# Kernel optimization log

Measured on AMD Instinct MI355X. Metric: run time of the kernel, lower is better.

Reference implementation:

```python
import jax, jax.numpy as jnp
import numpy as np

N_NODES = 50000
N_EDGES = 1600000
IN_CH = 128
OUT_CH = 128


def setup_inputs() -> dict:
    key = jax.random.key(0)
    k1, k2, k3, k4, k5 = jax.random.split(key, 5)
    x = jax.random.normal(k1, (N_NODES, IN_CH), dtype=jnp.float32)
    # edge_index[0] = destination (row), edge_index[1] = source (col)
    edge_index = jax.random.randint(k2, (2, N_EDGES), 0, N_NODES, dtype=jnp.int64)
    # Linear parameters (PyTorch default init: U(-1/sqrt(fan_in), 1/sqrt(fan_in)))
    bound = 1.0 / np.sqrt(IN_CH)
    W = jax.random.uniform(k3, (OUT_CH, IN_CH), dtype=jnp.float32, minval=-bound, maxval=bound)
    b = jax.random.uniform(k4, (OUT_CH,), dtype=jnp.float32, minval=-bound, maxval=bound)
    return {"x": x, "edge_index": edge_index, "W": W, "b": b}


def reference(x, edge_index, W, b) -> jnp.ndarray:
    # Linear projection: h = x @ W^T + b  -> [N, OUT_CH]
    h = jnp.einsum("nd,od->no", x, W) + b
    # spmm sum aggregation: out[dst] = sum_{edges e: dst(e)=dst} h[src(e)]
    dst = edge_index[0]
    src = edge_index[1]
    out = jax.ops.segment_sum(h[src], dst, num_segments=N_NODES)
    return out
```

## Files before the change

### kernel.cpp

```cpp
#include <hip/hip_runtime.h>

constexpr int N  = 50000;
constexpr int E  = 1600000;
constexpr int CH = 128;

constexpr int BSZ  = 64;
constexpr int NB   = (N + BSZ - 1) / BSZ;
constexpr int CAP  = 2560;
constexpr int PBLK = 256;
constexpr int EPB  = E / PBLK;
constexpr int GEMM_BLOCKS = N / 16;

constexpr size_t H_OFF     = 0;
constexpr size_t H_SZ      = (size_t)N * CH * 2;
constexpr size_t PAIRS_OFF = H_OFF + H_SZ;
constexpr size_t PAIRS_SZ  = (size_t)NB * CAP * 4;
constexpr size_t GCUR_OFF  = PAIRS_OFF + PAIRS_SZ;
constexpr size_t GCUR_SZ   = 3328;
constexpr size_t REQUIRED  = GCUR_OFF + GCUR_SZ;
constexpr size_t FB_REQUIRED = H_SZ;

static __device__ __forceinline__ ushort f2bf(float f) {
    unsigned u = __float_as_uint(f);
    return (ushort)((u + 0x7fffu + ((u >> 16) & 1u)) >> 16);
}
static __device__ __forceinline__ float bf_lo(unsigned u) { return __uint_as_float(u << 16); }
static __device__ __forceinline__ float bf_hi(unsigned u) { return __uint_as_float(u & 0xffff0000u); }

typedef __attribute__((ext_vector_type(8))) short bf16x8;
typedef __attribute__((ext_vector_type(4))) float f32x4;

static __device__ __forceinline__ void gemm_body(int gb, int tid,
                                                 const float* __restrict__ x,
                                                 const float* __restrict__ W,
                                                 const float* __restrict__ bias,
                                                 ushort* __restrict__ h) {
    const int m    = tid & 15;
    const int q    = (tid >> 4) & 3;
    const int wave = tid >> 6;
    const int r0   = gb * 16;
    const int c0   = wave * 32;

    const float* xrow = x + (size_t)(r0 + m) * CH + q * 8;
    const float* wr0  = W + (size_t)(c0 + m) * CH + q * 8;
    const float* wr1  = wr0 + 16 * CH;

    f32x4 acc0 = {0.f, 0.f, 0.f, 0.f};
    f32x4 acc1 = {0.f, 0.f, 0.f, 0.f};

#pragma unroll
    for (int kc = 0; kc < CH; kc += 32) {
        float4 xa = *(const float4*)(xrow + kc);
        float4 xb = *(const float4*)(xrow + kc + 4);
        float4 wa0 = *(const float4*)(wr0 + kc);
        float4 wb0 = *(const float4*)(wr0 + kc + 4);
        float4 wa1 = *(const float4*)(wr1 + kc);
        float4 wb1 = *(const float4*)(wr1 + kc + 4);
        bf16x8 a, b0, b1;
        a[0] = (short)f2bf(xa.x); a[1] = (short)f2bf(xa.y);
        a[2] = (short)f2bf(xa.z); a[3] = (short)f2bf(xa.w);
        a[4] = (short)f2bf(xb.x); a[5] = (short)f2bf(xb.y);
        a[6] = (short)f2bf(xb.z); a[7] = (short)f2bf(xb.w);
        b0[0] = (short)f2bf(wa0.x); b0[1] = (short)f2bf(wa0.y);
        b0[2] = (short)f2bf(wa0.z); b0[3] = (short)f2bf(wa0.w);
        b0[4] = (short)f2bf(wb0.x); b0[5] = (short)f2bf(wb0.y);
        b0[6] = (short)f2bf(wb0.z); b0[7] = (short)f2bf(wb0.w);
        b1[0] = (short)f2bf(wa1.x); b1[1] = (short)f2bf(wa1.y);
        b1[2] = (short)f2bf(wa1.z); b1[3] = (short)f2bf(wa1.w);
        b1[4] = (short)f2bf(wb1.x); b1[5] = (short)f2bf(wb1.y);
        b1[6] = (short)f2bf(wb1.z); b1[7] = (short)f2bf(wb1.w);
        acc0 = __builtin_amdgcn_mfma_f32_16x16x32_bf16(a, b0, acc0, 0, 0, 0);
        acc1 = __builtin_amdgcn_mfma_f32_16x16x32_bf16(a, b1, acc1, 0, 0, 0);
    }

    const int col0 = c0 + m;
    const float bb0 = bias[col0];
    const float bb1 = bias[col0 + 16];
#pragma unroll
    for (int r = 0; r < 4; r++) {
        size_t row = (size_t)(r0 + q * 4 + r) * CH;
        h[row + col0]      = f2bf(acc0[r] + bb0);
        h[row + col0 + 16] = f2bf(acc1[r] + bb1);
    }
}

__global__ __launch_bounds__(256) void gemm_and_scatter(const float* __restrict__ x,
                                                        const float* __restrict__ W,
                                                        const float* __restrict__ bias,
                                                        ushort* __restrict__ h,
                                                        const int* __restrict__ ei,
                                                        int* __restrict__ gcur,
                                                        unsigned* __restrict__ pairs) {
    __shared__ unsigned raw[EPB];
    __shared__ ushort   srt16[EPB];
    __shared__ int cnt[NB];
    __shared__ int lstart[NB];
    __shared__ int gpos[NB];
    __shared__ int cur[NB];
    __shared__ int ssum[256];
    const int bid = blockIdx.x;
    const int tid = threadIdx.x;

    if (bid >= PBLK) {
        gemm_body(bid - PBLK, tid, x, W, bias, h);
        return;
    }

    const int k = bid;
    const int* dp = ei + k * EPB;
    const int* sp = ei + E + k * EPB;

    for (int j = tid; j < NB; j += 256) cnt[j] = 0;
    for (int i = tid; i < EPB; i += 256) {
        int d = dp[i], s = sp[i];
        raw[i] = ((unsigned)(d >> 6) << 22) | ((unsigned)(d & (BSZ - 1)) << 16) | (unsigned)s;
    }
    __syncthreads();

    for (int i = tid; i < EPB; i += 256) atomicAdd(&cnt[raw[i] >> 22], 1);
    __syncthreads();

    for (int j = tid; j < NB; j += 256) {
        int c = cnt[j];
        gpos[j] = j * CAP + (c ? atomicAdd(&gcur[j], c) : 0);
    }

    {
        const int base = tid * 4;
        int s = 0;
#pragma unroll
        for (int i = 0; i < 4; i++) { int j = base + i; if (j < NB) s += cnt[j]; }
        ssum[tid] = s;
        __syncthreads();
        for (int o = 1; o < 256; o <<= 1) {
            int u = (tid >= o) ? ssum[tid - o] : 0;
            __syncthreads();
            ssum[tid] += u;
            __syncthreads();
        }
        int run = ssum[tid] - s;
#pragma unroll
        for (int i = 0; i < 4; i++) {
            int j = base + i;
            if (j < NB) { lstart[j] = run; cur[j] = run; run += cnt[j]; }
        }
    }
    __syncthreads();

    for (int i = tid; i < EPB; i += 256) {
        int p = atomicAdd(&cur[raw[i] >> 22], 1);
        srt16[p] = (ushort)i;
    }
    __syncthreads();

    for (int i = tid; i < EPB; i += 256) {
        unsigned w = raw[srt16[i]];
        int bkt = w >> 22;
        int gdst = gpos[bkt] + (i - lstart[bkt]);
        if (gdst < (bkt + 1) * CAP)
            pairs[gdst] = w;
    }
}

__global__ __launch_bounds__(512) void agg_fused(const ushort* __restrict__ h,
                                                 const unsigned* __restrict__ pairs,
                                                 const int* __restrict__ gcur,
                                                 float* __restrict__ out) {
    __shared__ unsigned raw[CAP];
    __shared__ ushort   srt[CAP];
    __shared__ int hist[BSZ], offs[BSZ], cur[BSZ];
    const int b = blockIdx.x, t = threadIdx.x;
    const int cnt = min(gcur[b], CAP);
    const int wave = t >> 6;
    const int lane = t & 63;
    const int quarter = lane >> 4;
    const int cq      = lane & 15;

    const unsigned* slab = pairs + (size_t)b * CAP;
    for (int i = t; i < cnt; i += 512) raw[i] = slab[i];
    if (t < BSZ) hist[t] = 0;
    __syncthreads();
    for (int i = t; i < cnt; i += 512) atomicAdd(&hist[(raw[i] >> 16) & (BSZ - 1)], 1);
    __syncthreads();
    int v = (t < BSZ) ? hist[t] : 0;
    if (t < BSZ) offs[t] = v;
    __syncthreads();
    for (int o = 1; o < BSZ; o <<= 1) {
        int u = 0;
        if (t < BSZ && t >= o) u = offs[t - o];
        __syncthreads();
        if (t < BSZ) offs[t] += u;
        __syncthreads();
    }
    if (t < BSZ) { int excl = offs[t] - v; offs[t] = excl; cur[t] = excl; }
    __syncthreads();
    for (int i = t; i < cnt; i += 512) {
        unsigned w = raw[i];
        int p = atomicAdd(&cur[(w >> 16) & (BSZ - 1)], 1);
        srt[p] = (ushort)(w & 0xffffu);
    }
    __syncthreads();

    const ushort* hp = h + (size_t)cq * 8;

#pragma unroll
    for (int j = 0; j < 8; j++) {
        const int nl = wave * 8 + j;
        const int st = offs[nl];
        const int c  = hist[nl];
        float a0 = 0.f, a1 = 0.f, a2 = 0.f, a3 = 0.f;
        float a4 = 0.f, a5 = 0.f, a6 = 0.f, a7 = 0.f;
        int i = 0;
        for (; i + 16 <= c; i += 16) {
            const int e0 = st + i + quarter;
            int s0 = srt[e0];
            int s1 = srt[e0 + 4];
            int s2 = srt[e0 + 8];
            int s3 = srt[e0 + 12];
            uint4 v0 = *(const uint4*)(hp + (size_t)s0 * CH);
            uint4 v1 = *(const uint4*)(hp + (size_t)s1 * CH);
            uint4 v2 = *(const uint4*)(hp + (size_t)s2 * CH);
            uint4 v3 = *(const uint4*)(hp + (size_t)s3 * CH);
            a0 += bf_lo(v0.x); a1 += bf_hi(v0.x); a2 += bf_lo(v0.y); a3 += bf_hi(v0.y);
            a4 += bf_lo(v0.z); a5 += bf_hi(v0.z); a6 += bf_lo(v0.w); a7 += bf_hi(v0.w);
            a0 += bf_lo(v1.x); a1 += bf_hi(v1.x); a2 += bf_lo(v1.y); a3 += bf_hi(v1.y);
            a4 += bf_lo(v1.z); a5 += bf_hi(v1.z); a6 += bf_lo(v1.w); a7 += bf_hi(v1.w);
            a0 += bf_lo(v2.x); a1 += bf_hi(v2.x); a2 += bf_lo(v2.y); a3 += bf_hi(v2.y);
            a4 += bf_lo(v2.z); a5 += bf_hi(v2.z); a6 += bf_lo(v2.w); a7 += bf_hi(v2.w);
            a0 += bf_lo(v3.x); a1 += bf_hi(v3.x); a2 += bf_lo(v3.y); a3 += bf_hi(v3.y);
            a4 += bf_lo(v3.z); a5 += bf_hi(v3.z); a6 += bf_lo(v3.w); a7 += bf_hi(v3.w);
        }
        for (; i < c; i += 4) {
            if (i + quarter < c) {
                int s = srt[st + i + quarter];
                uint4 vv = *(const uint4*)(hp + (size_t)s * CH);
                a0 += bf_lo(vv.x); a1 += bf_hi(vv.x); a2 += bf_lo(vv.y); a3 += bf_hi(vv.y);
                a4 += bf_lo(vv.z); a5 += bf_hi(vv.z); a6 += bf_lo(vv.w); a7 += bf_hi(vv.w);
            }
        }
        a0 += __shfl_xor(a0, 16); a0 += __shfl_xor(a0, 32);
        a1 += __shfl_xor(a1, 16); a1 += __shfl_xor(a1, 32);
        a2 += __shfl_xor(a2, 16); a2 += __shfl_xor(a2, 32);
        a3 += __shfl_xor(a3, 16); a3 += __shfl_xor(a3, 32);
        a4 += __shfl_xor(a4, 16); a4 += __shfl_xor(a4, 32);
        a5 += __shfl_xor(a5, 16); a5 += __shfl_xor(a5, 32);
        a6 += __shfl_xor(a6, 16); a6 += __shfl_xor(a6, 32);
        a7 += __shfl_xor(a7, 16); a7 += __shfl_xor(a7, 32);
        const int n = b * BSZ + nl;
        if (quarter == 0 && n < N) {
            float* op = out + (size_t)n * CH + cq * 8;
            *(float4*)(op)     = make_float4(a0, a1, a2, a3);
            *(float4*)(op + 4) = make_float4(a4, a5, a6, a7);
        }
    }
}

__global__ __launch_bounds__(256) void gemm_only(const float* __restrict__ x,
                                                 const float* __restrict__ W,
                                                 const float* __restrict__ bias,
                                                 ushort* __restrict__ h) {
    gemm_body(blockIdx.x, threadIdx.x, x, W, bias, h);
}

__global__ void atomic_agg(const ushort* __restrict__ h, const int* __restrict__ ei,
                           float* __restrict__ out) {
    int tid = blockIdx.x * blockDim.x + threadIdx.x;
    int e  = tid >> 5;
    int cg = (tid & 31) * 4;
    if (e < E) {
        int d = ei[e];
        int s = ei[E + e];
        ushort4 v = *(const ushort4*)(h + (size_t)s * CH + cg);
        float* o = out + (size_t)d * CH + cg;
        atomicAdd(o + 0, __uint_as_float((unsigned)v.x << 16));
        atomicAdd(o + 1, __uint_as_float((unsigned)v.y << 16));
        atomicAdd(o + 2, __uint_as_float((unsigned)v.z << 16));
        atomicAdd(o + 3, __uint_as_float((unsigned)v.w << 16));
    }
}

extern "C" void kernel_launch(void* const* d_in, const int* in_sizes, int n_in,
                              void* d_out, int out_size, void* d_ws, size_t ws_size,
                              hipStream_t stream) {
    const float* x  = (const float*)d_in[0];
    const int*   ei = (const int*)d_in[1];
    const float* W  = (const float*)d_in[2];
    const float* b  = (const float*)d_in[3];
    float* out = (float*)d_out;

    char* ws = (char*)d_ws;
    ushort* h = (ushort*)(ws + H_OFF);

    if (ws_size >= REQUIRED) {
        unsigned* pairs = (unsigned*)(ws + PAIRS_OFF);
        int*      gcur  = (int*)(ws + GCUR_OFF);

        hipMemsetAsync(gcur, 0, NB * sizeof(int), stream);
        gemm_and_scatter<<<PBLK + GEMM_BLOCKS, 256, 0, stream>>>(x, W, b, h, ei, gcur, pairs);
        agg_fused<<<NB, 512, 0, stream>>>(h, pairs, gcur, out);
    } else if (ws_size >= FB_REQUIRED) {
        gemm_only<<<GEMM_BLOCKS, 256, 0, stream>>>(x, W, b, h);
        hipMemsetAsync(out, 0, (size_t)out_size * sizeof(float), stream);
        int total = E * 32;
        atomic_agg<<<(total + 255) / 256, 256, 0, stream>>>(h, ei, out);
    }
}
```

Baseline: 178.7 us.

## Sort aggregation edges by source quarter and use 1024-thread blocks

The aggregation kernel now sorts each bucket's edges by destination and also by which quarter of the source-node range they come from. All waves sweep quarter 0 first, then quarter 1, and so on, carrying accumulators across passes. The aim is to keep the concurrently gathered h rows in a smaller working set for better L2/cache locality. The block size doubles to 1024 threads with 4 nodes per wave, which adds a partially unrolled 8-edge loop and more registers for the accumulators. In exchange it adds a larger scan, more barrier steps, and possible occupancy pressure.

```diff
diff --git a/kernel.cpp b/kernel.cpp
--- a/kernel.cpp
+++ b/kernel.cpp
@@ -9,7 +9,9 @@
 constexpr int CAP  = 2560;
 constexpr int PBLK = 256;
 constexpr int EPB  = E / PBLK;
-constexpr int GEMM_BLOCKS = N / 16;
+constexpr int GEMM_TILES = N / 16;
+constexpr int NQ   = 4;
+constexpr int NKEY = BSZ * NQ;
 
 constexpr size_t H_OFF     = 0;
 constexpr size_t H_SZ      = (size_t)N * CH * 2;
@@ -162,13 +164,13 @@
     }
 }
 
-__global__ __launch_bounds__(512) void agg_fused(const ushort* __restrict__ h,
-                                                 const unsigned* __restrict__ pairs,
-                                                 const int* __restrict__ gcur,
-                                                 float* __restrict__ out) {
+__global__ __launch_bounds__(1024) void agg_fused(const ushort* __restrict__ h,
+                                                  const unsigned* __restrict__ pairs,
+                                                  const int* __restrict__ gcur,
+                                                  float* __restrict__ out) {
     __shared__ unsigned raw[CAP];
     __shared__ ushort   srt[CAP];
-    __shared__ int hist[BSZ], offs[BSZ], cur[BSZ];
+    __shared__ int hist[NKEY], offs[NKEY], cur[NKEY];
     const int b = blockIdx.x, t = threadIdx.x;
     const int cnt = min(gcur[b], CAP);
     const int wave = t >> 6;
@@ -177,67 +179,101 @@
     const int cq      = lane & 15;
 
     const unsigned* slab = pairs + (size_t)b * CAP;
-    for (int i = t; i < cnt; i += 512) raw[i] = slab[i];
-    if (t < BSZ) hist[t] = 0;
-    __syncthreads();
-    for (int i = t; i < cnt; i += 512) atomicAdd(&hist[(raw[i] >> 16) & (BSZ - 1)], 1);
-    __syncthreads();
-    int v = (t < BSZ) ? hist[t] : 0;
-    if (t < BSZ) offs[t] = v;
-    __syncthreads();
-    for (int o = 1; o < BSZ; o <<= 1) {
+    for (int i = t; i < cnt; i += 1024) raw[i] = slab[i];
+    if (t < NKEY) hist[t] = 0;
+    __syncthreads();
+    for (int i = t; i < cnt; i += 1024) {
+        unsigned w = raw[i];
+        int key = (((w >> 16) & (BSZ - 1)) << 2) | ((w & 0xffffu) / 12500u);
+        atomicAdd(&hist[key], 1);
+    }
+    __syncthreads();
+    int v = (t < NKEY) ? hist[t] : 0;
+    if (t < NKEY) offs[t] = v;
+    __syncthreads();
+    for (int o = 1; o < NKEY; o <<= 1) {
         int u = 0;
-        if (t < BSZ && t >= o) u = offs[t - o];
+        if (t < NKEY && t >= o) u = offs[t - o];
         __syncthreads();
-        if (t < BSZ) offs[t] += u;
+        if (t < NKEY) offs[t] += u;
         __syncthreads();
     }
-    if (t < BSZ) { int excl = offs[t] - v; offs[t] = excl; cur[t] = excl; }
-    __syncthreads();
-    for (int i = t; i < cnt; i += 512) {
+    if (t < NKEY) { int excl = offs[t] - v; offs[t] = excl; cur[t] = excl; }
+    __syncthreads();
+    for (int i = t; i < cnt; i += 1024) {
         unsigned w = raw[i];
-        int p = atomicAdd(&cur[(w >> 16) & (BSZ - 1)], 1);
+        int key = (((w >> 16) & (BSZ - 1)) << 2) | ((w & 0xffffu) / 12500u);
+        int p = atomicAdd(&cur[key], 1);
         srt[p] = (ushort)(w & 0xffffu);
     }
     __syncthreads();
 
     const ushort* hp = h + (size_t)cq * 8;
 
-#pragma unroll
-    for (int j = 0; j < 8; j++) {
-        const int nl = wave * 8 + j;
-        const int st = offs[nl];
-        const int c  = hist[nl];
-        float a0 = 0.f, a1 = 0.f, a2 = 0.f, a3 = 0.f;
-        float a4 = 0.f, a5 = 0.f, a6 = 0.f, a7 = 0.f;
-        int i = 0;
-        for (; i + 16 <= c; i += 16) {
-            const int e0 = st + i + quarter;
-            int s0 = srt[e0];
-            int s1 = srt[e0 + 4];
-            int s2 = srt[e0 + 8];
-            int s3 = srt[e0 + 12];
-            uint4 v0 = *(const uint4*)(hp + (size_t)s0 * CH);
-            uint4 v1 = *(const uint4*)(hp + (size_t)s1 * CH);
-            uint4 v2 = *(const uint4*)(hp + (size_t)s2 * CH);
-            uint4 v3 = *(const uint4*)(hp + (size_t)s3 * CH);
-            a0 += bf_lo(v0.x); a1 += bf_hi(v0.x); a2 += bf_lo(v0.y); a3 += bf_hi(v0.y);
-            a4 += bf_lo(v0.z); a5 += bf_hi(v0.z); a6 += bf_lo(v0.w); a7 += bf_hi(v0.w);
-            a0 += bf_lo(v1.x); a1 += bf_hi(v1.x); a2 += bf_lo(v1.y); a3 += bf_hi(v1.y);
-            a4 += bf_lo(v1.z); a5 += bf_hi(v1.z); a6 += bf_lo(v1.w); a7 += bf_hi(v1.w);
-            a0 += bf_lo(v2.x); a1 += bf_hi(v2.x); a2 += bf_lo(v2.y); a3 += bf_hi(v2.y);
-            a4 += bf_lo(v2.z); a5 += bf_hi(v2.z); a6 += bf_lo(v2.w); a7 += bf_hi(v2.w);
-            a0 += bf_lo(v3.x); a1 += bf_hi(v3.x); a2 += bf_lo(v3.y); a3 += bf_hi(v3.y);
-            a4 += bf_lo(v3.z); a5 += bf_hi(v3.z); a6 += bf_lo(v3.w); a7 += bf_hi(v3.w);
+    float acc[4][8];
+#pragma unroll
+    for (int j = 0; j < 4; j++)
+#pragma unroll
+        for (int z = 0; z < 8; z++) acc[j][z] = 0.f;
+
+#pragma unroll
+    for (int q = 0; q < NQ; q++) {
+#pragma unroll
+        for (int j = 0; j < 4; j++) {
+            const int nl = wave * 4 + j;
+            const int key = (nl << 2) | q;
+            const int st = offs[key];
+            const int c  = hist[key];
+            float a0 = acc[j][0], a1 = acc[j][1], a2 = acc[j][2], a3 = acc[j][3];
+            float a4 = acc[j][4], a5 = acc[j][5], a6 = acc[j][6], a7 = acc[j][7];
+            int i = 0;
+            for (; i + 16 <= c; i += 16) {
+                const int e0 = st + i + quarter;
+                int s0 = srt[e0];
+                int s1 = srt[e0 + 4];
+                int s2 = srt[e0 + 8];
+                int s3 = srt[e0 + 12];
+                uint4 v0 = *(const uint4*)(hp + (size_t)s0 * CH);
+                uint4 v1 = *(const uint4*)(hp + (size_t)s1 * CH);
+                uint4 v2 = *(const uint4*)(hp + (size_t)s2 * CH);
+                uint4 v3 = *(const uint4*)(hp + (size_t)s3 * CH);
+                a0 += bf_lo(v0.x); a1 += bf_hi(v0.x); a2 += bf_lo(v0.y); a3 += bf_hi(v0.y);
+                a4 += bf_lo(v0.z); a5 += bf_hi(v0.z); a6 += bf_lo(v0.w); a7 += bf_hi(v0.w);
+                a0 += bf_lo(v1.x); a1 += bf_hi(v1.x); a2 += bf_lo(v1.y); a3 += bf_hi(v1.y);
+                a4 += bf_lo(v1.z); a5 += bf_hi(v1.z); a6 += bf_lo(v1.w); a7 += bf_hi(v1.w);
+                a0 += bf_lo(v2.x); a1 += bf_hi(v2.x); a2 += bf_lo(v2.y); a3 += bf_hi(v2.y);
+                a4 += bf_lo(v2.z); a5 += bf_hi(v2.z); a6 += bf_lo(v2.w); a7 += bf_hi(v2.w);
+                a0 += bf_lo(v3.x); a1 += bf_hi(v3.x); a2 += bf_lo(v3.y); a3 += bf_hi(v3.y);
+                a4 += bf_lo(v3.z); a5 += bf_hi(v3.z); a6 += bf_lo(v3.w); a7 += bf_hi(v3.w);
+            }
+            for (; i + 8 <= c; i += 8) {
+                const int e0 = st + i + quarter;
+                int s0 = srt[e0];
+                int s1 = srt[e0 + 4];
+                uint4 v0 = *(const uint4*)(hp + (size_t)s0 * CH);
+                uint4 v1 = *(const uint4*)(hp + (size_t)s1 * CH);
+                a0 += bf_lo(v0.x); a1 += bf_hi(v0.x); a2 += bf_lo(v0.y); a3 += bf_hi(v0.y);
+                a4 += bf_lo(v0.z); a5 += bf_hi(v0.z); a6 += bf_lo(v0.w); a7 += bf_hi(v0.w);
+                a0 += bf_lo(v1.x); a1 += bf_hi(v1.x); a2 += bf_lo(v1.y); a3 += bf_hi(v1.y);
+                a4 += bf_lo(v1.z); a5 += bf_hi(v1.z); a6 += bf_lo(v1.w); a7 += bf_hi(v1.w);
+            }
+            for (; i < c; i += 4) {
+                if (i + quarter < c) {
+                    int s = srt[st + i + quarter];
+                    uint4 vv = *(const uint4*)(hp + (size_t)s * CH);
+                    a0 += bf_lo(vv.x); a1 += bf_hi(vv.x); a2 += bf_lo(vv.y); a3 += bf_hi(vv.y);
+                    a4 += bf_lo(vv.z); a5 += bf_hi(vv.z); a6 += bf_lo(vv.w); a7 += bf_hi(vv.w);
+                }
+            }
+            acc[j][0] = a0; acc[j][1] = a1; acc[j][2] = a2; acc[j][3] = a3;
+            acc[j][4] = a4; acc[j][5] = a5; acc[j][6] = a6; acc[j][7] = a7;
         }
-        for (; i < c; i += 4) {
-            if (i + quarter < c) {
-                int s = srt[st + i + quarter];
-                uint4 vv = *(const uint4*)(hp + (size_t)s * CH);
-                a0 += bf_lo(vv.x); a1 += bf_hi(vv.x); a2 += bf_lo(vv.y); a3 += bf_hi(vv.y);
-                a4 += bf_lo(vv.z); a5 += bf_hi(vv.z); a6 += bf_lo(vv.w); a7 += bf_hi(vv.w);
-            }
-        }
+    }
+
+#pragma unroll
+    for (int j = 0; j < 4; j++) {
+        float a0 = acc[j][0], a1 = acc[j][1], a2 = acc[j][2], a3 = acc[j][3];
+        float a4 = acc[j][4], a5 = acc[j][5], a6 = acc[j][6], a7 = acc[j][7];
         a0 += __shfl_xor(a0, 16); a0 += __shfl_xor(a0, 32);
         a1 += __shfl_xor(a1, 16); a1 += __shfl_xor(a1, 32);
         a2 += __shfl_xor(a2, 16); a2 += __shfl_xor(a2, 32);
@@ -246,7 +282,7 @@
         a5 += __shfl_xor(a5, 16); a5 += __shfl_xor(a5, 32);
         a6 += __shfl_xor(a6, 16); a6 += __shfl_xor(a6, 32);
         a7 += __shfl_xor(a7, 16); a7 += __shfl_xor(a7, 32);
-        const int n = b * BSZ + nl;
+        const int n = b * BSZ + wave * 4 + j;
         if (quarter == 0 && n < N) {
             float* op = out + (size_t)n * CH + cq * 8;
             *(float4*)(op)     = make_float4(a0, a1, a2, a3);
@@ -296,10 +332,10 @@
         int*      gcur  = (int*)(ws + GCUR_OFF);
 
         hipMemsetAsync(gcur, 0, NB * sizeof(int), stream);
-        gemm_and_scatter<<<PBLK + GEMM_BLOCKS, 256, 0, stream>>>(x, W, b, h, ei, gcur, pairs);
-        agg_fused<<<NB, 512, 0, stream>>>(h, pairs, gcur, out);
+        gemm_and_scatter<<<PBLK + GEMM_TILES, 256, 0, stream>>>(x, W, b, h, ei, gcur, pairs);
+        agg_fused<<<NB, 1024, 0, stream>>>(h, pairs, gcur, out);
     } else if (ws_size >= FB_REQUIRED) {
-        gemm_only<<<GEMM_BLOCKS, 256, 0, stream>>>(x, W, b, h);
+        gemm_only<<<GEMM_TILES, 256, 0, stream>>>(x, W, b, h);
         hipMemsetAsync(out, 0, (size_t)out_size * sizeof(float), stream);
         int total = E * 32;
         atomic_agg<<<(total + 255) / 256, 256, 0, stream>>>(h, ei, out);
```

Measured after the change: 198.6 us. 1.11x slower.
